# Kernel tuning notes

Measured on AMD Instinct MI355X. Metric: run time of the kernel, lower is better.

## Reference

```python
import jax, jax.numpy as jnp
import numpy as np

B, L, H, V, G, TGB = 128, 512, 256, 100000, 4, 128
S = 2 * L - 1  # max_sequence_tokens = 2*history_capacity - 1


def setup_inputs() -> dict:
    key = jax.random.key(0)
    ks = jax.random.split(key, 16)
    d = {}
    d['history_tokens'] = jax.random.randint(ks[0], (B, L), 0, V)
    d['history_post_tokens'] = jax.random.randint(ks[1], (B, L), 0, V)
    d['history_author_tokens'] = jax.random.randint(ks[2], (B, L), 0, V)
    d['history_action_tokens'] = jax.random.randint(ks[3], (B, L), 0, V)
    d['history_time_gap'] = jax.random.randint(ks[4], (B, L), 0, TGB + 1)
    d['history_group_ids'] = jnp.sort(jax.random.randint(ks[5], (B, L), 0, G + 1), axis=-1)
    d['lengths'] = jax.random.randint(ks[6], (B,), 0, L + 1)
    # embedding tables (padding_idx=0 rows zeroed as in nn.Embedding(padding_idx=0))
    d['token_table'] = (jax.random.normal(ks[7], (V, H)) * 0.02).at[0].set(0.0)
    d['time_table'] = (jax.random.normal(ks[8], (TGB + 1, H)) * 0.02).at[0].set(0.0)
    d['group_table'] = (jax.random.normal(ks[9], (G + 1, H)) * 0.02).at[0].set(0.0)
    d['pos_table'] = jax.random.normal(ks[10], (S, H)) * 0.02
    d['sep_token'] = jax.random.normal(ks[11], (H,)) * 0.02
    # event_projection params: LayerNorm(6H) -> Linear(6H,4H) -> SiLU -> Linear(4H,H)
    d['ln_gamma'] = jnp.ones((6 * H,), jnp.float32)
    d['ln_beta'] = jnp.zeros((6 * H,), jnp.float32)
    d['W1'] = jax.random.normal(ks[12], (6 * H, 4 * H)) * (1.0 / np.sqrt(6 * H))
    d['b1'] = jnp.zeros((4 * H,), jnp.float32)
    d['W2'] = jax.random.normal(ks[13], (4 * H, H)) * (1.0 / np.sqrt(4 * H))
    d['b2'] = jnp.zeros((H,), jnp.float32)
    return d


def _layernorm(x, g, b, eps=1e-5):
    m = x.mean(-1, keepdims=True)
    v = x.var(-1, keepdims=True)
    return (x - m) / jnp.sqrt(v + eps) * g + b


def reference(history_tokens, history_post_tokens, history_author_tokens,
              history_action_tokens, history_time_gap, history_group_ids,
              lengths, token_table, time_table, group_table, pos_table,
              sep_token, ln_gamma, ln_beta, W1, b1, W2, b2):
    # --- event embedding: 6 lookups concat -> LN -> MLP  (dropout is eval no-op)
    ev = jnp.concatenate([
        token_table[history_tokens],
        token_table[history_post_tokens],
        token_table[history_author_tokens],
        token_table[history_action_tokens],
        time_table[jnp.clip(history_time_gap, 0, TGB)],
        group_table[history_group_ids],
    ], axis=-1)  # [B, L, 6H]
    h = _layernorm(ev, ln_gamma, ln_beta)
    h = jax.nn.silu(h @ W1 + b1)
    event = h @ W2 + b2  # [B, L, H]

    # --- vectorized merge_with_sep (ragged right-aligned pack with sep at group boundaries)
    pos = jnp.arange(L)
    mask = pos[None, :] < lengths[:, None]                       # prefix validity mask
    gid_next = jnp.concatenate([history_group_ids[:, 1:], history_group_ids[:, -1:]], axis=1)
    boundary = (pos[None, :] < lengths[:, None] - 1) & (history_group_ids != gid_next)
    ex = jnp.cumsum(boundary, axis=1) - boundary                 # seps strictly before event p
    event_idx = pos[None, :] + ex                                # piece index of event p
    M = lengths + boundary.sum(axis=1)                           # total pieces per row
    shift = S - M                                                # may be negative (left-truncate)
    pos_e = shift[:, None] + event_idx
    pos_s = pos_e + 1
    valid_e = mask & (pos_e >= 0)
    valid_s = boundary & (pos_s >= 0)
    barange = jnp.arange(B)[:, None]
    buf = jnp.zeros((B, S + 1, H), event.dtype)                  # extra slot S = trash bin
    buf = buf.at[barange, jnp.where(valid_e, pos_e, S)].set(
        jnp.where(valid_e[..., None], event, 0.0))
    buf = buf.at[barange, jnp.where(valid_s, pos_s, S)].set(
        jnp.where(valid_s[..., None], sep_token, 0.0))
    merged = buf[:, :S]
    merged_mask = jnp.arange(S)[None, :] >= jnp.maximum(shift, 0)[:, None]
    merged = (merged + pos_table[None]) * merged_mask[..., None].astype(merged.dtype)
    return merged, merged_mask
```

## Files before the change

kernel.cpp:

```cpp
#include <hip/hip_runtime.h>

#define B_    128
#define L_    512
#define H_    256
#define TGB_  128
#define S_    1023
#define BL_   (B_ * L_)
#define SIXH  1536
#define FOURH 1024

typedef __bf16 bf16_t;
typedef bf16_t bf16x8 __attribute__((ext_vector_type(8)));
typedef float  f32x4  __attribute__((ext_vector_type(4)));
typedef unsigned short u16x4 __attribute__((ext_vector_type(4)));

template<int P> struct IC { static constexpr int v = P; };

__device__ __forceinline__ unsigned short f2bf(float f) {
    union { float f; unsigned u; } v; v.f = f;
    unsigned u = v.u;
    unsigned r = u + 0x7FFFu + ((u >> 16) & 1u);
    return (unsigned short)(r >> 16);
}

__device__ __forceinline__ void gload_lds16(const void* g, void* l) {
    __builtin_amdgcn_global_load_lds(
        (__attribute__((address_space(1))) void*)(void*)(g),
        (__attribute__((address_space(3))) void*)(l), 16, 0, 0);
}

__global__ __launch_bounds__(256) void transpose_bf16_kernel(
    const float* __restrict__ in, unsigned short* __restrict__ out,
    int R, int C)
{
    __shared__ float tile[32][33];
    int rb = blockIdx.x * 32, cb = blockIdx.y * 32;
    int tx = threadIdx.x & 31, ty = threadIdx.x >> 5;
    #pragma unroll
    for (int d = 0; d < 32; d += 8)
        tile[ty + d][tx] = in[(size_t)(rb + ty + d) * C + cb + tx];
    __syncthreads();
    #pragma unroll
    for (int d = 0; d < 32; d += 8)
        out[(size_t)(cb + ty + d) * R + rb + tx] = f2bf(tile[tx][ty + d]);
}

__global__ __launch_bounds__(256) void embed_ln_kernel(
    const int* __restrict__ tok,  const int* __restrict__ ptok,
    const int* __restrict__ atok, const int* __restrict__ actok,
    const int* __restrict__ tgap, const int* __restrict__ gid,
    const float* __restrict__ ttab, const float* __restrict__ titab,
    const float* __restrict__ gtab, const float* __restrict__ gamma,
    const float* __restrict__ beta, const int* __restrict__ row_id,
    const int* __restrict__ Vdev, unsigned short* __restrict__ xln)
{
    int j = blockIdx.x * 4 + (threadIdx.x >> 6);
    if (j >= *Vdev) return;
    int l = threadIdx.x & 63;
    int rid = row_id[j];
    int i0 = tok[rid], i1 = ptok[rid], i2 = atok[rid], i3 = actok[rid];
    int i4 = tgap[rid]; i4 = i4 < 0 ? 0 : (i4 > TGB_ ? TGB_ : i4);
    int i5 = gid[rid];
    f32x4 v[6];
    v[0] = *(const f32x4*)(ttab  + (size_t)i0 * H_ + l * 4);
    v[1] = *(const f32x4*)(ttab  + (size_t)i1 * H_ + l * 4);
    v[2] = *(const f32x4*)(ttab  + (size_t)i2 * H_ + l * 4);
    v[3] = *(const f32x4*)(ttab  + (size_t)i3 * H_ + l * 4);
    v[4] = *(const f32x4*)(titab + (size_t)i4 * H_ + l * 4);
    v[5] = *(const f32x4*)(gtab  + (size_t)i5 * H_ + l * 4);
    float s = 0.0f, sq = 0.0f;
    #pragma unroll
    for (int k = 0; k < 6; ++k)
        #pragma unroll
        for (int c = 0; c < 4; ++c) { float f = v[k][c]; s += f; sq += f * f; }
    #pragma unroll
    for (int off = 32; off > 0; off >>= 1) {
        s  += __shfl_xor(s,  off);
        sq += __shfl_xor(sq, off);
    }
    float mean = s * (1.0f / 1536.0f);
    float var  = sq * (1.0f / 1536.0f) - mean * mean;
    float rstd = rsqrtf(var + 1e-5f);
    unsigned short* orow = xln + (size_t)j * SIXH;
    #pragma unroll
    for (int k = 0; k < 6; ++k) {
        f32x4 g = *(const f32x4*)(gamma + k * H_ + l * 4);
        f32x4 b = *(const f32x4*)(beta  + k * H_ + l * 4);
        u16x4 o;
        #pragma unroll
        for (int c = 0; c < 4; ++c)
            o[c] = f2bf((v[k][c] - mean) * rstd * g[c] + b[c]);
        *(u16x4*)(orow + k * H_ + l * 4) = o;
    }
}

__global__ __launch_bounds__(512, 2) void gemm1_kernel(
    const unsigned short* __restrict__ A,
    const unsigned short* __restrict__ Bt,
    const float* __restrict__ bias,
    unsigned short* __restrict__ C,
    const int* __restrict__ Vdev)
{
    constexpr int N = FOURH, K = SIXH, NTN = 4;
    constexpr int NT = K / 64;
    constexpr int IT = NT / 2;
    extern __shared__ __align__(16) unsigned short lds[];

    const int V = *Vdev;
    const int nact = ((V + 255) >> 8) * NTN;
    const int q = nact >> 3, r = nact & 7;

    const int t = threadIdx.x;
    const int w = t >> 6, l = t & 63;
    const int wm = w >> 2, wn = w & 3;
    const int r16 = l & 15, ql = l >> 4;
    const int sg = (t & 3) ^ ((t >> 3) & 3);
    unsigned short* ldsb = lds + w * 512;
    const int fr = (ql ^ ((r16 >> 1) & 3)) * 8;

    for (int bidv = blockIdx.x; bidv < nact; bidv += 512) {
        const int x = bidv & 7, o = bidv >> 3;
        const int wid = (x < r ? x * (q + 1) : r * (q + 1) + (x - r) * q) + o;
        const int mt  = wid / NTN;
        const int m0  = mt * 256;
        const int n0  = (wid - mt * NTN) * 256;

        const unsigned short* As0 = A  + (size_t)(m0 + (t >> 2)) * K + sg * 8;
        const unsigned short* As1 = As0 + (size_t)128 * K;
        const unsigned short* Bs0 = Bt + (size_t)(n0 + (t >> 2)) * K + sg * 8;
        const unsigned short* Bs1 = Bs0 + (size_t)128 * K;
        const unsigned short* la0 = lds + (wm * 128 + r16) * 32 + fr;
        const unsigned short* la1 = la0 + 32768;
        const unsigned short* lb0 = lds + 16384 + (wn * 64 + r16) * 32 + fr;
        const unsigned short* lb1 = lb0 + 32768;

        f32x4 acc[8][4];
        #pragma unroll
        for (int i = 0; i < 8; ++i)
            #pragma unroll
            for (int j = 0; j < 4; ++j) acc[i][j] = (f32x4)0.0f;

        auto ST2 = [&](const unsigned short* s0, const unsigned short* s1,
                       int dofs, int gofs) {
            gload_lds16(s0 + gofs, ldsb + dofs);
            gload_lds16(s1 + gofs, ldsb + dofs + 4096);
        };

        if (bidv != (int)blockIdx.x) __syncthreads();

        ST2(As0, As1, 0,     0);
        ST2(Bs0, Bs1, 16384, 0);
        ST2(As0, As1, 8192,  32);
        ST2(Bs0, Bs1, 24576, 32);
        ST2(As0, As1, 32768, 64);
        ST2(Bs0, Bs1, 49152, 64);
        asm volatile("s_waitcnt vmcnt(4)\ns_barrier" ::: "memory");

        bf16x8 bq[4];

        auto phase = [&](auto pc, bool last) {
            constexpr int P   = decltype(pc)::v;
            constexpr int BUF = P >> 2;
            constexpr int KK  = (P & 3) >> 1;
            constexpr int MH  = P & 1;
            const unsigned short* ab = (BUF ? la1 : la0) + KK * 8192 + MH * 2048;
            bf16x8 aq[4];
            if constexpr (MH == 0) {
                const unsigned short* bb = (BUF ? lb1 : lb0) + KK * 8192;
                bq[0] = *(const bf16x8*)(bb);
                bq[1] = *(const bf16x8*)(bb + 512);
                bq[2] = *(const bf16x8*)(bb + 1024);
                bq[3] = *(const bf16x8*)(bb + 1536);
            }
            aq[0] = *(const bf16x8*)(ab);
            aq[1] = *(const bf16x8*)(ab + 512);
            aq[2] = *(const bf16x8*)(ab + 1024);
            aq[3] = *(const bf16x8*)(ab + 1536);
            if constexpr (P == 0)      {            ST2(As0, As1, 40960, 96);  }
            else if constexpr (P == 1) {            ST2(Bs0, Bs1, 57344, 96);  }
            else if constexpr (P == 2) { if (!last) ST2(As0, As1, 0,     128); }
            else if constexpr (P == 3) { if (!last) ST2(Bs0, Bs1, 16384, 128); }
            else if constexpr (P == 4) { if (!last) ST2(As0, As1, 8192,  160); }
            else if constexpr (P == 5) { if (!last) ST2(Bs0, Bs1, 24576, 160); }
            else if constexpr (P == 6) { if (!last) ST2(As0, As1, 32768, 192); }
            else                       { if (!last) ST2(Bs0, Bs1, 49152, 192); }
            asm volatile("s_barrier" ::: "memory");
            __builtin_amdgcn_s_setprio(1);
            #pragma unroll
            for (int mm = 0; mm < 4; ++mm)
                #pragma unroll
                for (int nn = 0; nn < 4; ++nn)
                    acc[MH * 4 + mm][nn] = __builtin_amdgcn_mfma_f32_16x16x32_bf16(
                        aq[mm], bq[nn], acc[MH * 4 + mm][nn], 0, 0, 0);
            __builtin_amdgcn_s_setprio(0);
            if constexpr (P == 3) {
                if (last) asm volatile("s_waitcnt vmcnt(0)\ns_barrier" ::: "memory");
                else      asm volatile("s_waitcnt vmcnt(4)\ns_barrier" ::: "memory");
            } else if constexpr (P == 7) {
                if (!last) asm volatile("s_waitcnt vmcnt(4)\ns_barrier" ::: "memory");
            } else {
                asm volatile("s_barrier" ::: "memory");
            }
        };

        for (int it = 0; it < IT; ++it) {
            const bool last = (it == IT - 1);
            phase(IC<0>{}, last);
            phase(IC<1>{}, last);
            phase(IC<2>{}, last);
            phase(IC<3>{}, last);
            phase(IC<4>{}, last);
            phase(IC<5>{}, last);
            phase(IC<6>{}, last);
            phase(IC<7>{}, last);
            As0 += 128; As1 += 128; Bs0 += 128; Bs1 += 128;
        }

        #pragma unroll
        for (int mi = 0; mi < 8; ++mi) {
            #pragma unroll
            for (int ni = 0; ni < 4; ++ni) {
                int col = n0 + wn * 64 + ni * 16 + r16;
                float bv = bias[col];
                #pragma unroll
                for (int j = 0; j < 4; ++j) {
                    int row = m0 + wm * 128 + mi * 16 + ql * 4 + j;
                    float v = acc[mi][ni][j] + bv;
                    v = v / (1.0f + __expf(-v));
                    C[(size_t)row * N + col] = f2bf(v);
                }
            }
        }
    }
}

__global__ __launch_bounds__(512, 2) void gemm2_kernel(
    const unsigned short* __restrict__ A,
    const unsigned short* __restrict__ Bt,
    const float* __restrict__ bias,
    const int* __restrict__ outslot,
    const int* __restrict__ posC,
    const float* __restrict__ ptab,
    float* __restrict__ outF,
    const int* __restrict__ Vdev)
{
    constexpr int K = FOURH, NT = K / 64;
    constexpr int ASLOT = 256 * 64;
    constexpr int BSLOT = 128 * 64;
    extern __shared__ __align__(16) unsigned short lds[];
    unsigned short* sA = lds;
    unsigned short* sB = lds + 3 * ASLOT;

    const int V = *Vdev;
    const int nact = ((V + 255) >> 8) * 2;
    const int bid = blockIdx.x;
    if (bid >= nact) return;
    const int qd = nact >> 3, rd = nact & 7, x = bid & 7, o = bid >> 3;
    const int wid = (x < rd ? x * (qd + 1) : rd * (qd + 1) + (x - rd) * qd) + o;
    const int m0 = (wid >> 1) * 256;
    const int n0 = (wid & 1) * 128;

    int t = threadIdx.x;
    int w = t >> 6, l = t & 63;
    int srow = t >> 3;
    int scg  = (t & 7) ^ (srow & 7);
    const unsigned short* Ag = A  + (size_t)(m0 + srow) * K + scg * 8;
    const unsigned short* Bg = Bt + (size_t)(n0 + srow) * K + scg * 8;
    unsigned short* stA = sA + w * 512;
    unsigned short* stB = sB + w * 512;

    int r16 = l & 15, q = l >> 4;
    int wm = w >> 1, wn = w & 1;
    int xr = r16 & 7;
    const int aoff = (wm * 64 + r16) * 64;
    const int boff = (wn * 64 + r16) * 64;
    const int c0 = ((0 + q) ^ xr) * 8;
    const int c1 = ((4 + q) ^ xr) * 8;

    f32x4 acc[4][4];
    #pragma unroll
    for (int i = 0; i < 4; ++i)
        #pragma unroll
        for (int j = 0; j < 4; ++j) acc[i][j] = (f32x4)0.0f;

    #pragma unroll
    for (int j = 0; j < 4; ++j) gload_lds16(Ag + (size_t)j * 64 * K, stA + j * 4096);
    #pragma unroll
    for (int j = 0; j < 2; ++j) gload_lds16(Bg + (size_t)j * 64 * K, stB + j * 4096);
    #pragma unroll
    for (int j = 0; j < 4; ++j) gload_lds16(Ag + (size_t)j * 64 * K + 64, stA + ASLOT + j * 4096);
    #pragma unroll
    for (int j = 0; j < 2; ++j) gload_lds16(Bg + (size_t)j * 64 * K + 64, stB + BSLOT + j * 4096);
    asm volatile("s_waitcnt vmcnt(6)\ns_barrier" ::: "memory");

    int s = 0;
    for (int kt = 0; kt < NT; ++kt) {
        const unsigned short* sAs = sA + s * ASLOT;
        const unsigned short* sBs = sB + s * BSLOT;
        int spf = s + 2; if (spf >= 3) spf -= 3;
        const size_t gofs = (size_t)(kt + 2) * 64;
        unsigned short* pA = stA + spf * ASLOT;
        unsigned short* pB = stB + spf * BSLOT;

        bf16x8 af[4][2];
        #pragma unroll
        for (int mi = 0; mi < 4; ++mi) {
            af[mi][0] = *(const bf16x8*)(sAs + aoff + mi * 1024 + c0);
            af[mi][1] = *(const bf16x8*)(sAs + aoff + mi * 1024 + c1);
        }
        #pragma unroll
        for (int ni = 0; ni < 4; ++ni) {
            bf16x8 b0 = *(const bf16x8*)(sBs + boff + ni * 1024 + c0);
            bf16x8 b1 = *(const bf16x8*)(sBs + boff + ni * 1024 + c1);
            if (kt + 2 < NT) {
                if (ni == 0) {
                    gload_lds16(Ag + gofs,                    pA);
                    gload_lds16(Ag + (size_t) 64 * K + gofs,  pA + 4096);
                } else if (ni == 1) {
                    gload_lds16(Ag + (size_t)128 * K + gofs,  pA + 8192);
                    gload_lds16(Ag + (size_t)192 * K + gofs,  pA + 12288);
                } else if (ni == 2) {
                    gload_lds16(Bg + gofs,                    pB);
                } else {
                    gload_lds16(Bg + (size_t) 64 * K + gofs,  pB + 4096);
                }
            }
            __builtin_amdgcn_s_setprio(1);
            #pragma unroll
            for (int mi = 0; mi < 4; ++mi) {
                acc[mi][ni] = __builtin_amdgcn_mfma_f32_16x16x32_bf16(af[mi][0], b0, acc[mi][ni], 0, 0, 0);
                acc[mi][ni] = __builtin_amdgcn_mfma_f32_16x16x32_bf16(af[mi][1], b1, acc[mi][ni], 0, 0, 0);
            }
            __builtin_amdgcn_s_setprio(0);
        }
        if (kt + 2 < NT)      asm volatile("s_waitcnt vmcnt(6)\ns_barrier" ::: "memory");
        else if (kt + 1 < NT) asm volatile("s_waitcnt vmcnt(0)\ns_barrier" ::: "memory");
        s = (s == 2) ? 0 : s + 1;
    }

    #pragma unroll
    for (int mi = 0; mi < 4; ++mi) {
        #pragma unroll
        for (int j = 0; j < 4; ++j) {
            int row = m0 + wm * 64 + mi * 16 + q * 4 + j;
            int slot = outslot[row];
            if (slot >= 0) {
                float* orow = outF + (size_t)slot * H_;
                const float* prow = ptab + (size_t)posC[row] * H_;
                #pragma unroll
                for (int ni = 0; ni < 4; ++ni) {
                    int col = n0 + wn * 64 + ni * 16 + r16;
                    orow[col] = acc[mi][ni][j] + bias[col] + prow[col];
                }
            }
        }
    }
}

__global__ __launch_bounds__(512) void scan_scatter_kernel(
    const int* __restrict__ gid, const int* __restrict__ lengths,
    int* __restrict__ idx_map, int* __restrict__ shiftb,
    int* __restrict__ row_id, int* __restrict__ outslot,
    int* __restrict__ posC, int* __restrict__ Vdev)
{
    int b = blockIdx.x, i = threadIdx.x;
    __shared__ int slen[128];
    __shared__ int sres[2];
    if (i < 128) slen[i] = lengths[i];
    __syncthreads();
    if (i < 64) {
        int vpart = (i < b ? slen[i] : 0) + (i + 64 < b ? slen[i + 64] : 0);
        int vall  = slen[i] + slen[i + 64];
        #pragma unroll
        for (int off = 32; off > 0; off >>= 1) {
            vpart += __shfl_xor(vpart, off);
            vall  += __shfl_xor(vall,  off);
        }
        if (i == 0) { sres[0] = vpart; sres[1] = vall; }
    }
    int len = lengths[b];
    int g  = gid[b * L_ + i];
    int gn = (i < L_ - 1) ? gid[b * L_ + i + 1] : g;
    int bnd = (i < len - 1 && g != gn) ? 1 : 0;
    __shared__ int sc[512];
    sc[i] = bnd;
    __syncthreads();
    for (int off = 1; off < 512; off <<= 1) {
        int v = (i >= off) ? sc[i - off] : 0;
        __syncthreads();
        sc[i] += v;
        __syncthreads();
    }
    int incl  = sc[i];
    int total = sc[511];
    int ex = incl - bnd;
    int M = len + total;
    int shift = S_ - M;
    int pb = sres[0], V = sres[1];
    for (int s = i; s < S_; s += 512) idx_map[b * S_ + s] = -1;
    __syncthreads();
    if (i < len) {
        int p = shift + i + ex;
        idx_map[b * S_ + p] = i;
        if (bnd) idx_map[b * S_ + p + 1] = -2;
        int j = pb + i;
        row_id[j]  = b * L_ + i;
        outslot[j] = b * S_ + p;
        posC[j]    = p;
    }
    if (i == 0) shiftb[b] = shift;
    if (b == B_ - 1) {
        if (i == 0) *Vdev = V;
        if (i < 256) outslot[V + i] = -1;
    }
}

__global__ __launch_bounds__(256) void fill_kernel(
    const int* __restrict__ idx_map, const int* __restrict__ shiftb,
    const float* __restrict__ ptab, const float* __restrict__ sep,
    float* __restrict__ out)
{
    int b = blockIdx.y;
    int s = blockIdx.x * 4 + (threadIdx.x >> 6);
    if (s >= S_) return;
    int h = (threadIdx.x & 63) * 4;
    int shift = shiftb[b];
    float* orow = out + ((size_t)b * S_ + s) * H_;
    if (s < shift) {
        *(f32x4*)(orow + h) = (f32x4)0.0f;
    } else {
        int idx = idx_map[b * S_ + s];
        if (idx == -2) {
            f32x4 pv = *(const f32x4*)(ptab + (size_t)s * H_ + h);
            f32x4 sv = *(const f32x4*)(sep + h);
            *(f32x4*)(orow + h) = pv + sv;
        }
    }
    if ((threadIdx.x & 63) == 0)
        out[(size_t)B_ * S_ * H_ + (size_t)b * S_ + s] = (s >= shift) ? 1.0f : 0.0f;
}

extern "C" void kernel_launch(void* const* d_in, const int* in_sizes, int n_in,
                              void* d_out, int out_size, void* d_ws, size_t ws_size,
                              hipStream_t stream)
{
    const int*   tok   = (const int*)d_in[0];
    const int*   ptok  = (const int*)d_in[1];
    const int*   atok  = (const int*)d_in[2];
    const int*   actok = (const int*)d_in[3];
    const int*   tgap  = (const int*)d_in[4];
    const int*   gid   = (const int*)d_in[5];
    const int*   lens  = (const int*)d_in[6];
    const float* ttab  = (const float*)d_in[7];
    const float* titab = (const float*)d_in[8];
    const float* gtab  = (const float*)d_in[9];
    const float* post  = (const float*)d_in[10];
    const float* sep   = (const float*)d_in[11];
    const float* gamma = (const float*)d_in[12];
    const float* beta  = (const float*)d_in[13];
    const float* W1    = (const float*)d_in[14];
    const float* b1    = (const float*)d_in[15];
    const float* W2    = (const float*)d_in[16];
    const float* b2    = (const float*)d_in[17];

    unsigned short* xln  = (unsigned short*)d_ws;
    unsigned short* hbuf = xln  + (size_t)BL_ * SIXH;
    unsigned short* W1T  = hbuf + (size_t)BL_ * FOURH;
    unsigned short* W2T  = W1T  + (size_t)FOURH * SIXH;
    int* idx_map = (int*)(W2T + (size_t)H_ * FOURH);
    int* shiftb  = idx_map + B_ * S_;
    int* Vdev    = shiftb + B_;
    int* row_id  = Vdev + 4;
    int* outslot = row_id + BL_;
    int* posC    = outslot + BL_ + 256;
    float* out   = (float*)d_out;

    constexpr int LDS1 = 2 * 32768 * 2;
    constexpr int LDS2 = 3 * (256 * 64 + 128 * 64) * 2;
    (void)hipFuncSetAttribute((const void*)&gemm1_kernel,
                              hipFuncAttributeMaxDynamicSharedMemorySize, LDS1);
    (void)hipFuncSetAttribute((const void*)&gemm2_kernel,
                              hipFuncAttributeMaxDynamicSharedMemorySize, LDS2);

    transpose_bf16_kernel<<<dim3(SIXH / 32, FOURH / 32), 256, 0, stream>>>(W1, W1T, SIXH, FOURH);
    transpose_bf16_kernel<<<dim3(FOURH / 32, H_ / 32),   256, 0, stream>>>(W2, W2T, FOURH, H_);

    scan_scatter_kernel<<<B_, 512, 0, stream>>>(gid, lens, idx_map, shiftb,
                                                row_id, outslot, posC, Vdev);

    embed_ln_kernel<<<BL_ / 4, 256, 0, stream>>>(tok, ptok, atok, actok, tgap, gid,
                                                 ttab, titab, gtab, gamma, beta,
                                                 row_id, Vdev, xln);

    gemm1_kernel<<<512, 512, LDS1, stream>>>(xln, W1T, b1, hbuf, Vdev);
    gemm2_kernel<<<512, 512, LDS2, stream>>>(hbuf, W2T, b2, outslot, posC, post, out, Vdev);

    fill_kernel<<<dim3((S_ + 3) / 4, B_), 256, 0, stream>>>(idx_map, shiftb, post, sep, out);
}
```

Before: 282.4 us.

## Swap GEMM tilings: 256x128 3-stage for GEMM1, 128x128 persistent for GEMM2

GEMM1 (SiLU MLP layer) now runs on the former GEMM2 design, templated: 256x128 tiles, 3-stage LDS ring, one tile per block, 2048 blocks. GEMM2 (output projection plus scatter) now uses a new persistent 128x128-tile kernel with 256 threads and a double-buffered 8-phase pipeline, so the narrow N=256 GEMM gets more tiles and better CU fill. The aim is better occupancy and load balance for both GEMMs, at the cost of lower arithmetic intensity per tile in GEMM2.

```diff
diff --git a/kernel.cpp b/kernel.cpp
--- a/kernel.cpp
+++ b/kernel.cpp
@@ -94,157 +94,15 @@
     }
 }
 
-__global__ __launch_bounds__(512, 2) void gemm1_kernel(
+template<int N, int K, int NTN>
+__global__ __launch_bounds__(512, 2) void gemm8_kernel(
     const unsigned short* __restrict__ A,
     const unsigned short* __restrict__ Bt,
     const float* __restrict__ bias,
     unsigned short* __restrict__ C,
     const int* __restrict__ Vdev)
 {
-    constexpr int N = FOURH, K = SIXH, NTN = 4;
     constexpr int NT = K / 64;
-    constexpr int IT = NT / 2;
-    extern __shared__ __align__(16) unsigned short lds[];
-
-    const int V = *Vdev;
-    const int nact = ((V + 255) >> 8) * NTN;
-    const int q = nact >> 3, r = nact & 7;
-
-    const int t = threadIdx.x;
-    const int w = t >> 6, l = t & 63;
-    const int wm = w >> 2, wn = w & 3;
-    const int r16 = l & 15, ql = l >> 4;
-    const int sg = (t & 3) ^ ((t >> 3) & 3);
-    unsigned short* ldsb = lds + w * 512;
-    const int fr = (ql ^ ((r16 >> 1) & 3)) * 8;
-
-    for (int bidv = blockIdx.x; bidv < nact; bidv += 512) {
-        const int x = bidv & 7, o = bidv >> 3;
-        const int wid = (x < r ? x * (q + 1) : r * (q + 1) + (x - r) * q) + o;
-        const int mt  = wid / NTN;
-        const int m0  = mt * 256;
-        const int n0  = (wid - mt * NTN) * 256;
-
-        const unsigned short* As0 = A  + (size_t)(m0 + (t >> 2)) * K + sg * 8;
-        const unsigned short* As1 = As0 + (size_t)128 * K;
-        const unsigned short* Bs0 = Bt + (size_t)(n0 + (t >> 2)) * K + sg * 8;
-        const unsigned short* Bs1 = Bs0 + (size_t)128 * K;
-        const unsigned short* la0 = lds + (wm * 128 + r16) * 32 + fr;
-        const unsigned short* la1 = la0 + 32768;
-        const unsigned short* lb0 = lds + 16384 + (wn * 64 + r16) * 32 + fr;
-        const unsigned short* lb1 = lb0 + 32768;
-
-        f32x4 acc[8][4];
-        #pragma unroll
-        for (int i = 0; i < 8; ++i)
-            #pragma unroll
-            for (int j = 0; j < 4; ++j) acc[i][j] = (f32x4)0.0f;
-
-        auto ST2 = [&](const unsigned short* s0, const unsigned short* s1,
-                       int dofs, int gofs) {
-            gload_lds16(s0 + gofs, ldsb + dofs);
-            gload_lds16(s1 + gofs, ldsb + dofs + 4096);
-        };
-
-        if (bidv != (int)blockIdx.x) __syncthreads();
-
-        ST2(As0, As1, 0,     0);
-        ST2(Bs0, Bs1, 16384, 0);
-        ST2(As0, As1, 8192,  32);
-        ST2(Bs0, Bs1, 24576, 32);
-        ST2(As0, As1, 32768, 64);
-        ST2(Bs0, Bs1, 49152, 64);
-        asm volatile("s_waitcnt vmcnt(4)\ns_barrier" ::: "memory");
-
-        bf16x8 bq[4];
-
-        auto phase = [&](auto pc, bool last) {
-            constexpr int P   = decltype(pc)::v;
-            constexpr int BUF = P >> 2;
-            constexpr int KK  = (P & 3) >> 1;
-            constexpr int MH  = P & 1;
-            const unsigned short* ab = (BUF ? la1 : la0) + KK * 8192 + MH * 2048;
-            bf16x8 aq[4];
-            if constexpr (MH == 0) {
-                const unsigned short* bb = (BUF ? lb1 : lb0) + KK * 8192;
-                bq[0] = *(const bf16x8*)(bb);
-                bq[1] = *(const bf16x8*)(bb + 512);
-                bq[2] = *(const bf16x8*)(bb + 1024);
-                bq[3] = *(const bf16x8*)(bb + 1536);
-            }
-            aq[0] = *(const bf16x8*)(ab);
-            aq[1] = *(const bf16x8*)(ab + 512);
-            aq[2] = *(const bf16x8*)(ab + 1024);
-            aq[3] = *(const bf16x8*)(ab + 1536);
-            if constexpr (P == 0)      {            ST2(As0, As1, 40960, 96);  }
-            else if constexpr (P == 1) {            ST2(Bs0, Bs1, 57344, 96);  }
-            else if constexpr (P == 2) { if (!last) ST2(As0, As1, 0,     128); }
-            else if constexpr (P == 3) { if (!last) ST2(Bs0, Bs1, 16384, 128); }
-            else if constexpr (P == 4) { if (!last) ST2(As0, As1, 8192,  160); }
-            else if constexpr (P == 5) { if (!last) ST2(Bs0, Bs1, 24576, 160); }
-            else if constexpr (P == 6) { if (!last) ST2(As0, As1, 32768, 192); }
-            else                       { if (!last) ST2(Bs0, Bs1, 49152, 192); }
-            asm volatile("s_barrier" ::: "memory");
-            __builtin_amdgcn_s_setprio(1);
-            #pragma unroll
-            for (int mm = 0; mm < 4; ++mm)
-                #pragma unroll
-                for (int nn = 0; nn < 4; ++nn)
-                    acc[MH * 4 + mm][nn] = __builtin_amdgcn_mfma_f32_16x16x32_bf16(
-                        aq[mm], bq[nn], acc[MH * 4 + mm][nn], 0, 0, 0);
-            __builtin_amdgcn_s_setprio(0);
-            if constexpr (P == 3) {
-                if (last) asm volatile("s_waitcnt vmcnt(0)\ns_barrier" ::: "memory");
-                else      asm volatile("s_waitcnt vmcnt(4)\ns_barrier" ::: "memory");
-            } else if constexpr (P == 7) {
-                if (!last) asm volatile("s_waitcnt vmcnt(4)\ns_barrier" ::: "memory");
-            } else {
-                asm volatile("s_barrier" ::: "memory");
-            }
-        };
-
-        for (int it = 0; it < IT; ++it) {
-            const bool last = (it == IT - 1);
-            phase(IC<0>{}, last);
-            phase(IC<1>{}, last);
-            phase(IC<2>{}, last);
-            phase(IC<3>{}, last);
-            phase(IC<4>{}, last);
-            phase(IC<5>{}, last);
-            phase(IC<6>{}, last);
-            phase(IC<7>{}, last);
-            As0 += 128; As1 += 128; Bs0 += 128; Bs1 += 128;
-        }
-
-        #pragma unroll
-        for (int mi = 0; mi < 8; ++mi) {
-            #pragma unroll
-            for (int ni = 0; ni < 4; ++ni) {
-                int col = n0 + wn * 64 + ni * 16 + r16;
-                float bv = bias[col];
-                #pragma unroll
-                for (int j = 0; j < 4; ++j) {
-                    int row = m0 + wm * 128 + mi * 16 + ql * 4 + j;
-                    float v = acc[mi][ni][j] + bv;
-                    v = v / (1.0f + __expf(-v));
-                    C[(size_t)row * N + col] = f2bf(v);
-                }
-            }
-        }
-    }
-}
-
-__global__ __launch_bounds__(512, 2) void gemm2_kernel(
-    const unsigned short* __restrict__ A,
-    const unsigned short* __restrict__ Bt,
-    const float* __restrict__ bias,
-    const int* __restrict__ outslot,
-    const int* __restrict__ posC,
-    const float* __restrict__ ptab,
-    float* __restrict__ outF,
-    const int* __restrict__ Vdev)
-{
-    constexpr int K = FOURH, NT = K / 64;
     constexpr int ASLOT = 256 * 64;
     constexpr int BSLOT = 128 * 64;
     extern __shared__ __align__(16) unsigned short lds[];
@@ -252,13 +110,13 @@
     unsigned short* sB = lds + 3 * ASLOT;
 
     const int V = *Vdev;
-    const int nact = ((V + 255) >> 8) * 2;
+    const int nact = ((V + 255) >> 8) * NTN;
     const int bid = blockIdx.x;
     if (bid >= nact) return;
     const int qd = nact >> 3, rd = nact & 7, x = bid & 7, o = bid >> 3;
     const int wid = (x < rd ? x * (qd + 1) : rd * (qd + 1) + (x - rd) * qd) + o;
-    const int m0 = (wid >> 1) * 256;
-    const int n0 = (wid & 1) * 128;
+    const int m0 = (wid / NTN) * 256;
+    const int n0 = (wid % NTN) * 128;
 
     int t = threadIdx.x;
     int w = t >> 6, l = t & 63;
@@ -341,16 +199,158 @@
     #pragma unroll
     for (int mi = 0; mi < 4; ++mi) {
         #pragma unroll
-        for (int j = 0; j < 4; ++j) {
-            int row = m0 + wm * 64 + mi * 16 + q * 4 + j;
-            int slot = outslot[row];
-            if (slot >= 0) {
-                float* orow = outF + (size_t)slot * H_;
-                const float* prow = ptab + (size_t)posC[row] * H_;
+        for (int ni = 0; ni < 4; ++ni) {
+            int col = n0 + wn * 64 + ni * 16 + r16;
+            float bv = bias[col];
+            #pragma unroll
+            for (int j = 0; j < 4; ++j) {
+                int row = m0 + wm * 64 + mi * 16 + q * 4 + j;
+                float v = acc[mi][ni][j] + bv;
+                v = v / (1.0f + __expf(-v));
+                C[(size_t)row * N + col] = f2bf(v);
+            }
+        }
+    }
+}
+
+template<int K, int NTN>
+__global__ __launch_bounds__(256, 2) void gemm128s_kernel(
+    const unsigned short* __restrict__ A,
+    const unsigned short* __restrict__ Bt,
+    const float* __restrict__ bias,
+    const int* __restrict__ outslot,
+    const int* __restrict__ posC,
+    const float* __restrict__ ptab,
+    float* __restrict__ outF,
+    const int* __restrict__ Vdev)
+{
+    constexpr int NT = K / 64;
+    constexpr int IT = NT / 2;
+    extern __shared__ __align__(16) unsigned short lds[];
+
+    const int V = *Vdev;
+    const int nact = ((V + 127) >> 7) * NTN;
+    const int q = nact >> 3, r = nact & 7;
+
+    const int t = threadIdx.x;
+    const int w = t >> 6, l = t & 63;
+    const int wm = w >> 1, wn = w & 1;
+    const int r16 = l & 15, ql = l >> 4;
+    const int sg = (t & 3) ^ ((t >> 3) & 3);
+    unsigned short* ldsb = lds + w * 512;
+    const int fr = (ql ^ ((r16 >> 1) & 3)) * 8;
+
+    const unsigned short* la0 = lds + (wm * 64 + r16) * 32 + fr;
+    const unsigned short* la1 = la0 + 16384;
+    const unsigned short* lb0 = lds + 8192 + (wn * 64 + r16) * 32 + fr;
+    const unsigned short* lb1 = lb0 + 16384;
+
+    for (int bidv = blockIdx.x; bidv < nact; bidv += (int)gridDim.x) {
+        const int x = bidv & 7, o = bidv >> 3;
+        const int wid = (x < r ? x * (q + 1) : r * (q + 1) + (x - r) * q) + o;
+        const int mt  = wid / NTN;
+        const int m0  = mt * 128;
+        const int n0  = (wid - mt * NTN) * 128;
+
+        const unsigned short* As0 = A  + (size_t)(m0 + (t >> 2)) * K + sg * 8;
+        const unsigned short* As1 = As0 + (size_t)64 * K;
+        const unsigned short* Bs0 = Bt + (size_t)(n0 + (t >> 2)) * K + sg * 8;
+        const unsigned short* Bs1 = Bs0 + (size_t)64 * K;
+
+        f32x4 acc[4][4];
+        #pragma unroll
+        for (int i = 0; i < 4; ++i)
+            #pragma unroll
+            for (int j = 0; j < 4; ++j) acc[i][j] = (f32x4)0.0f;
+
+        auto ST2 = [&](const unsigned short* s0, const unsigned short* s1,
+                       int dofs, int gofs) {
+            gload_lds16(s0 + gofs, ldsb + dofs);
+            gload_lds16(s1 + gofs, ldsb + dofs + 2048);
+        };
+
+        if (bidv != (int)blockIdx.x) __syncthreads();
+
+        ST2(As0, As1, 0,     0);
+        ST2(Bs0, Bs1, 8192,  0);
+        ST2(As0, As1, 4096,  32);
+        ST2(Bs0, Bs1, 12288, 32);
+        ST2(As0, As1, 16384, 64);
+        ST2(Bs0, Bs1, 24576, 64);
+        asm volatile("s_waitcnt vmcnt(4)\ns_barrier" ::: "memory");
+
+        bf16x8 bq[4];
+
+        auto phase = [&](auto pc, bool last) {
+            constexpr int P   = decltype(pc)::v;
+            constexpr int BUF = P >> 2;
+            constexpr int KK  = (P & 3) >> 1;
+            constexpr int MH  = P & 1;
+            const unsigned short* ab = (BUF ? la1 : la0) + KK * 4096 + MH * 1024;
+            bf16x8 aq[2];
+            if constexpr (MH == 0) {
+                const unsigned short* bb = (BUF ? lb1 : lb0) + KK * 4096;
+                bq[0] = *(const bf16x8*)(bb);
+                bq[1] = *(const bf16x8*)(bb + 512);
+                bq[2] = *(const bf16x8*)(bb + 1024);
+                bq[3] = *(const bf16x8*)(bb + 1536);
+            }
+            aq[0] = *(const bf16x8*)(ab);
+            aq[1] = *(const bf16x8*)(ab + 512);
+            if constexpr (P == 0)      {            ST2(As0, As1, 20480, 96);  }
+            else if constexpr (P == 1) {            ST2(Bs0, Bs1, 28672, 96);  }
+            else if constexpr (P == 2) { if (!last) ST2(As0, As1, 0,     128); }
+            else if constexpr (P == 3) { if (!last) ST2(Bs0, Bs1, 8192,  128); }
+            else if constexpr (P == 4) { if (!last) ST2(As0, As1, 4096,  160); }
+            else if constexpr (P == 5) { if (!last) ST2(Bs0, Bs1, 12288, 160); }
+            else if constexpr (P == 6) { if (!last) ST2(As0, As1, 16384, 192); }
+            else                       { if (!last) ST2(Bs0, Bs1, 24576, 192); }
+            asm volatile("s_barrier" ::: "memory");
+            __builtin_amdgcn_s_setprio(1);
+            #pragma unroll
+            for (int mm = 0; mm < 2; ++mm)
                 #pragma unroll
-                for (int ni = 0; ni < 4; ++ni) {
-                    int col = n0 + wn * 64 + ni * 16 + r16;
-                    orow[col] = acc[mi][ni][j] + bias[col] + prow[col];
+                for (int nn = 0; nn < 4; ++nn)
+                    acc[MH * 2 + mm][nn] = __builtin_amdgcn_mfma_f32_16x16x32_bf16(
+                        aq[mm], bq[nn], acc[MH * 2 + mm][nn], 0, 0, 0);
+            __builtin_amdgcn_s_setprio(0);
+            if constexpr (P == 3) {
+                if (last) asm volatile("s_waitcnt vmcnt(0)\ns_barrier" ::: "memory");
+                else      asm volatile("s_waitcnt vmcnt(4)\ns_barrier" ::: "memory");
+            } else if constexpr (P == 7) {
+                if (!last) asm volatile("s_waitcnt vmcnt(4)\ns_barrier" ::: "memory");
+            } else {
+                asm volatile("s_barrier" ::: "memory");
+            }
+        };
+
+        for (int it = 0; it < IT; ++it) {
+            const bool last = (it == IT - 1);
+            phase(IC<0>{}, last);
+            phase(IC<1>{}, last);
+            phase(IC<2>{}, last);
+            phase(IC<3>{}, last);
+            phase(IC<4>{}, last);
+            phase(IC<5>{}, last);
+            phase(IC<6>{}, last);
+            phase(IC<7>{}, last);
+            As0 += 128; As1 += 128; Bs0 += 128; Bs1 += 128;
+        }
+
+        #pragma unroll
+        for (int mi = 0; mi < 4; ++mi) {
+            #pragma unroll
+            for (int j = 0; j < 4; ++j) {
+                int row = m0 + wm * 64 + mi * 16 + ql * 4 + j;
+                int slot = outslot[row];
+                if (slot >= 0) {
+                    float* orow = outF + (size_t)slot * H_;
+                    const float* prow = ptab + (size_t)posC[row] * H_;
+                    #pragma unroll
+                    for (int ni = 0; ni < 4; ++ni) {
+                        int col = n0 + wn * 64 + ni * 16 + r16;
+                        orow[col] = acc[mi][ni][j] + bias[col] + prow[col];
+                    }
                 }
             }
         }
@@ -475,11 +475,11 @@
     int* posC    = outslot + BL_ + 256;
     float* out   = (float*)d_out;
 
-    constexpr int LDS1 = 2 * 32768 * 2;
-    constexpr int LDS2 = 3 * (256 * 64 + 128 * 64) * 2;
-    (void)hipFuncSetAttribute((const void*)&gemm1_kernel,
+    constexpr int LDS1 = 3 * (256 * 64 + 128 * 64) * 2;
+    constexpr int LDS2 = 2 * 16384 * 2;
+    (void)hipFuncSetAttribute((const void*)&gemm8_kernel<FOURH, SIXH, 8>,
                               hipFuncAttributeMaxDynamicSharedMemorySize, LDS1);
-    (void)hipFuncSetAttribute((const void*)&gemm2_kernel,
+    (void)hipFuncSetAttribute((const void*)&gemm128s_kernel<FOURH, 2>,
                               hipFuncAttributeMaxDynamicSharedMemorySize, LDS2);
 
     transpose_bf16_kernel<<<dim3(SIXH / 32, FOURH / 32), 256, 0, stream>>>(W1, W1T, SIXH, FOURH);
@@ -492,8 +492,9 @@
                                                  ttab, titab, gtab, gamma, beta,
                                                  row_id, Vdev, xln);
 
-    gemm1_kernel<<<512, 512, LDS1, stream>>>(xln, W1T, b1, hbuf, Vdev);
-    gemm2_kernel<<<512, 512, LDS2, stream>>>(hbuf, W2T, b2, outslot, posC, post, out, Vdev);
+    gemm8_kernel<FOURH, SIXH, 8><<<2048, 512, LDS1, stream>>>(xln, W1T, b1, hbuf, Vdev);
+    gemm128s_kernel<FOURH, 2><<<1024, 256, LDS2, stream>>>(
+        hbuf, W2T, b2, outslot, posC, post, out, Vdev);
 
     fill_kernel<<<dim3((S_ + 3) / 4, B_), 256, 0, stream>>>(idx_map, shiftb, post, sep, out);
 }
```

Measured after the change: 274.0 us. 3.0% less time.
